# Performance work log

Hardware: AMD Instinct MI355X
Metric: run time of the kernel (lower is better)

Reference implementation:

```python
import jax, jax.numpy as jnp
import numpy as np

NUM_HEADS = 16
ROPE_THETA = 10000.0


def setup_inputs() -> dict:
    key = jax.random.key(0)
    k1, k2, k3 = jax.random.split(key, 3)
    B, S, D = 2, 2048, 1024
    std_qkv = float(np.sqrt(2.0 / (D + 3 * D)))
    std_out = float(np.sqrt(2.0 / (D + D)))
    return {
        "x": jax.random.normal(k1, (B, S, D), dtype=jnp.float32),
        "qkv_w": jax.random.normal(k2, (3 * D, D), dtype=jnp.float32) * std_qkv,
        "out_w": jax.random.normal(k3, (D, D), dtype=jnp.float32) * std_out,
        "token_positions": jnp.arange(S, dtype=jnp.int32),
    }


def _apply_rope(x, token_positions, theta=ROPE_THETA):
    # x: [B, H, S, d_k], token_positions: [S]
    d_k = x.shape[-1]
    inv_freqs = 1.0 / (theta ** (jnp.arange(0, d_k, 2, dtype=jnp.float32) / d_k))  # [d_k/2]
    angles = token_positions.astype(jnp.float32)[:, None] * inv_freqs[None, :]     # [S, d_k/2]
    cos, sin = jnp.cos(angles), jnp.sin(angles)
    x_even, x_odd = x[..., 0::2], x[..., 1::2]
    r_even = x_even * cos - x_odd * sin
    r_odd = x_even * sin + x_odd * cos
    # interleave back: [..., d_k/2, 2] -> [..., d_k]
    return jnp.stack([r_even, r_odd], axis=-1).reshape(x.shape)


def reference(x, qkv_w, out_w, token_positions):
    B, S, D = x.shape
    H = NUM_HEADS
    d_k = D // H

    qkv = jnp.einsum("bsd,ed->bse", x, qkv_w)                  # [B, S, 3*D]
    qkv = qkv.reshape(B, S, 3, H, d_k)
    q, k, v = (jnp.transpose(qkv[:, :, i], (0, 2, 1, 3)) for i in range(3))  # each [B, H, S, d_k]

    q = _apply_rope(q, token_positions)
    k = _apply_rope(k, token_positions)

    scale = 1.0 / jnp.sqrt(jnp.asarray(d_k, dtype=x.dtype))
    scores = jnp.einsum("bhqd,bhkd->bhqk", q, k) * scale       # [B, H, S, S]
    causal = jnp.tril(jnp.ones((S, S), dtype=bool))
    scores = jnp.where(causal, scores, jnp.asarray(-jnp.inf, dtype=scores.dtype))
    attn = jax.nn.softmax(scores, axis=-1)
    out = jnp.einsum("bhqk,bhkd->bhqd", attn, v)               # [B, H, S, d_k]
    out = jnp.transpose(out, (0, 2, 1, 3)).reshape(B, S, D)    # [B, S, D]
    return jnp.einsum("bsd,ed->bse", out, out_w)               # [B, S, D]
```

## Files before the change

### kernel.cpp

```cpp
#include <hip/hip_runtime.h>

typedef __bf16 bf16x8 __attribute__((ext_vector_type(8)));
typedef float f32x4 __attribute__((ext_vector_type(4)));
typedef unsigned short u16;
typedef u16 u16x8 __attribute__((ext_vector_type(8)));
typedef u16 u16x2 __attribute__((ext_vector_type(2)));

__device__ __forceinline__ u16 f2bf(float f) {
    union { float f; unsigned u; } x; x.f = f;
    unsigned r = x.u + 0x7fffu + ((x.u >> 16) & 1u);
    return (u16)(r >> 16);
}
__device__ __forceinline__ float bf2f(u16 v) {
    union { unsigned u; float f; } x; x.u = ((unsigned)v) << 16;
    return x.f;
}
__device__ __forceinline__ bf16x8 as_bf16x8(u16x8 v) {
    return __builtin_bit_cast(bf16x8, v);
}
__device__ __forceinline__ void glds16(const void* g, void* l) {
    __builtin_amdgcn_global_load_lds(
        (const __attribute__((address_space(1))) void*)g,
        (__attribute__((address_space(3))) void*)l, 16, 0, 0);
}
__device__ __forceinline__ int swz(int r) { return (((r & 7) ^ ((r >> 3) & 7)) << 3); }

__global__ __launch_bounds__(256) void cvt3(const float* __restrict__ x,
                                            const float* __restrict__ w,
                                            const float* __restrict__ ow,
                                            u16* __restrict__ x16,
                                            u16* __restrict__ w16,
                                            u16* __restrict__ ow16) {
    int i = blockIdx.x * 256 + threadIdx.x;
    const float* in; u16* out; int off;
    if (i < 524288)       { in = x;  out = x16;  off = i; }
    else if (i < 917504)  { in = w;  out = w16;  off = i - 524288; }
    else                  { in = ow; out = ow16; off = i - 917504; }
    const float4* p = (const float4*)(in + (size_t)off * 8);
    float4 a = p[0], b = p[1];
    u16x8 o;
    o[0] = f2bf(a.x); o[1] = f2bf(a.y); o[2] = f2bf(a.z); o[3] = f2bf(a.w);
    o[4] = f2bf(b.x); o[5] = f2bf(b.y); o[6] = f2bf(b.z); o[7] = f2bf(b.w);
    *(u16x8*)(out + (size_t)off * 8) = o;
}

__global__ __launch_bounds__(256) void gemm_qkv(const u16* __restrict__ A,
                                                const u16* __restrict__ B,
                                                u16* __restrict__ Qb,
                                                u16* __restrict__ Kb,
                                                u16* __restrict__ Vraw) {
    __shared__ u16 As[2][4096];
    __shared__ u16 Bs[2][4096];
    const int K = 1024, nbx = 24;
    const int tid = threadIdx.x, lane = tid & 63, wave = tid >> 6;
    const int cpx = gridDim.x >> 3;
    const int nid = (blockIdx.x & 7) * cpx + (blockIdx.x >> 3);
    const int m0 = (nid / nbx) << 7, n0 = (nid % nbx) << 7;
    const int wr = (wave >> 1) << 6, wc = (wave & 1) << 6;
    const int fr = lane & 15, fo = (lane >> 4) << 3;
    const int srow = tid >> 2, scol = (tid & 3) << 3;
    const u16* Ag = A + (size_t)(m0 + srow) * K + scol;
    const u16* Bg = B + (size_t)(n0 + srow) * K + scol;
    u16* AsW = &As[0][0] + (wave << 9);
    u16* BsW = &Bs[0][0] + (wave << 9);
    f32x4 acc[4][4] = {};
    const int nsteps = K >> 5;
    glds16(Ag, AsW);
    glds16(Ag + (size_t)64 * K, AsW + 2048);
    glds16(Bg, BsW);
    glds16(Bg + (size_t)64 * K, BsW + 2048);
    int cur = 0;
    for (int s = 0; s < nsteps; ++s) {
        __syncthreads();
        if (s + 1 < nsteps) {
            const u16* Ap = Ag + (s + 1) * 32;
            const u16* Bp = Bg + (s + 1) * 32;
            const int nb = (cur ^ 1) << 12;
            glds16(Ap, AsW + nb);
            glds16(Ap + (size_t)64 * K, AsW + nb + 2048);
            glds16(Bp, BsW + nb);
            glds16(Bp + (size_t)64 * K, BsW + nb + 2048);
        }
        const u16* Ab = &As[cur][0];
        const u16* Bb = &Bs[cur][0];
        bf16x8 af[4], bfr[4];
        #pragma unroll
        for (int i = 0; i < 4; ++i)
            af[i] = *(const bf16x8*)(Ab + (wr + i * 16 + fr) * 32 + fo);
        #pragma unroll
        for (int i = 0; i < 4; ++i)
            bfr[i] = *(const bf16x8*)(Bb + (wc + i * 16 + fr) * 32 + fo);
        #pragma unroll
        for (int i = 0; i < 4; ++i)
            #pragma unroll
            for (int j = 0; j < 4; ++j)
                acc[i][j] = __builtin_amdgcn_mfma_f32_16x16x32_bf16(af[i], bfr[j], acc[i][j], 0, 0, 0);
        cur ^= 1;
    }
    const int cr = (lane >> 4) << 2, cc = lane & 15;
    if (n0 >= 2048) {
        #pragma unroll
        for (int i = 0; i < 4; ++i)
            for (int j = 0; j < 4; ++j)
                for (int r = 0; r < 4; ++r)
                    Vraw[(size_t)(m0 + wr + i * 16 + cr + r) * 1024 +
                         (n0 - 2048 + wc + j * 16 + cc)] = f2bf(acc[i][j][r]);
    } else {
        const bool isQ = (n0 < 1024);
        u16* const Out = isQ ? Qb : Kb;
        const float qs = isQ ? 0.18033688011112042f : 1.0f;
        const float sgn = (cc & 1) ? 1.f : -1.f;
        const int bb = m0 >> 11;
        const int s_base = (m0 & 2047) + wr + cr;
        #pragma unroll
        for (int j = 0; j < 4; ++j) {
            const int n = n0 + wc + j * 16 + cc;
            const int d = n & 63, h = (n >> 6) & 15;
            const float invf = exp2f((float)(d >> 1) * -0.4152410118609203f)
                             * 0.15915494309189535f;
            u16* const ob = Out + (((size_t)(bb * 16 + h)) << 17) + d;
            #pragma unroll
            for (int i = 0; i < 4; ++i) {
                #pragma unroll
                for (int r = 0; r < 4; ++r) {
                    const int s = s_base + i * 16 + r;
                    float own  = acc[i][j][r];
                    float part = __shfl_xor(own, 1);
                    float rev  = (float)s * invf;
                    rev -= floorf(rev);
                    float sn = __builtin_amdgcn_sinf(rev);
                    float cs = __builtin_amdgcn_cosf(rev);
                    float o  = (cs * own + sgn * sn * part) * qs;
                    ob[(size_t)s * 64] = f2bf(o);
                }
            }
        }
    }
}

__global__ __launch_bounds__(256) void gemm128(const u16* __restrict__ A,
                                               const u16* __restrict__ B,
                                               float* __restrict__ C,
                                               int N, int K, int nbx) {
    __shared__ u16 As[2][4096];
    __shared__ u16 Bs[2][4096];
    const int tid = threadIdx.x, lane = tid & 63, wave = tid >> 6;
    const int cpx = gridDim.x >> 3;
    const int nid = (blockIdx.x & 7) * cpx + (blockIdx.x >> 3);
    const int m0 = (nid / nbx) << 7, n0 = (nid % nbx) << 7;
    const int wr = (wave >> 1) << 6, wc = (wave & 1) << 6;
    const int fr = lane & 15, fo = (lane >> 4) << 3;
    const int srow = tid >> 2, scol = (tid & 3) << 3;
    const u16* Ag = A + (size_t)(m0 + srow) * K + scol;
    const u16* Bg = B + (size_t)(n0 + srow) * K + scol;
    u16* AsW = &As[0][0] + (wave << 9);
    u16* BsW = &Bs[0][0] + (wave << 9);
    f32x4 acc[4][4] = {};
    const int nsteps = K >> 5;
    glds16(Ag, AsW);
    glds16(Ag + (size_t)64 * K, AsW + 2048);
    glds16(Bg, BsW);
    glds16(Bg + (size_t)64 * K, BsW + 2048);
    int cur = 0;
    for (int s = 0; s < nsteps; ++s) {
        __syncthreads();
        if (s + 1 < nsteps) {
            const u16* Ap = Ag + (s + 1) * 32;
            const u16* Bp = Bg + (s + 1) * 32;
            const int nb = (cur ^ 1) << 12;
            glds16(Ap, AsW + nb);
            glds16(Ap + (size_t)64 * K, AsW + nb + 2048);
            glds16(Bp, BsW + nb);
            glds16(Bp + (size_t)64 * K, BsW + nb + 2048);
        }
        const u16* Ab = &As[cur][0];
        const u16* Bb = &Bs[cur][0];
        bf16x8 af[4], bfr[4];
        #pragma unroll
        for (int i = 0; i < 4; ++i)
            af[i] = *(const bf16x8*)(Ab + (wr + i * 16 + fr) * 32 + fo);
        #pragma unroll
        for (int i = 0; i < 4; ++i)
            bfr[i] = *(const bf16x8*)(Bb + (wc + i * 16 + fr) * 32 + fo);
        #pragma unroll
        for (int i = 0; i < 4; ++i)
            #pragma unroll
            for (int j = 0; j < 4; ++j)
                acc[i][j] = __builtin_amdgcn_mfma_f32_16x16x32_bf16(af[i], bfr[j], acc[i][j], 0, 0, 0);
        cur ^= 1;
    }
    const int cr = (lane >> 4) << 2, cc = lane & 15;
    #pragma unroll
    for (int i = 0; i < 4; ++i)
        for (int j = 0; j < 4; ++j)
            for (int r = 0; r < 4; ++r)
                C[(size_t)(m0 + wr + i * 16 + cr + r) * N + (n0 + wc + j * 16 + cc)] =
                    acc[i][j][r];
}

__global__ __launch_bounds__(256) void vtrans(const u16* __restrict__ Vraw,
                                              u16* __restrict__ Vt) {
    __shared__ u16 lds[64][72];
    const int t = threadIdx.x;
    const int st = blockIdx.x, h = blockIdx.y, b = blockIdx.z;
    const int s0 = st << 6;
    {
        const int r = t >> 2, c0 = (t & 3) << 4;
        const u16* src = Vraw + (size_t)((b << 11) + s0 + r) * 1024 + h * 64 + c0;
        *(u16x8*)&lds[r][c0]     = *(const u16x8*)src;
        *(u16x8*)&lds[r][c0 + 8] = *(const u16x8*)(src + 8);
    }
    __syncthreads();
    const size_t obase = ((size_t)((b << 4) + h) << 17) + (st << 6);
    #pragma unroll
    for (int w = 0; w < 2; ++w) {
        const int q = t + (w << 8);
        const int d = q >> 3, c = q & 7;
        u16x8 o;
        #pragma unroll
        for (int i = 0; i < 8; ++i) {
            const int p = (c << 3) + i;
            const int k = ((p >> 5) << 5) + (((p >> 3) & 3) << 2) + (p & 3)
                        + (((p >> 2) & 1) << 4);
            o[i] = lds[k][d];
        }
        *(u16x8*)(Vt + obase + ((size_t)d << 11) + (c << 3)) = o;
    }
}

__global__ __launch_bounds__(512, 4) void attn_causal(const u16* __restrict__ Q,
                                                      const u16* __restrict__ K,
                                                      const u16* __restrict__ Vt,
                                                      u16* __restrict__ O) {
    __shared__ u16 smem[24576];
    __shared__ float cmb[5120];
    const int tid = threadIdx.x, lane = tid & 63, wave = tid >> 6;
    const int nid = ((blockIdx.x & 7) << 6) + (blockIdx.x >> 3);
    const int pr = nid & 15, h = (nid >> 4) & 15, b = nid >> 8;
    const int S = 2048;
    const size_t base = (size_t)((b << 4) + h) << 17;
    const int fr = lane & 15, fo = (lane >> 4) << 3, cr = (lane >> 4) << 2;
    const int schk = lane & 7, srow8 = lane >> 3;
    const int qsub = wave >> 1, half = wave & 1;
    float* const slot = cmb + qsub * 1280 + lane * 20;
    u16x8 ones_u;
    #pragma unroll
    for (int i = 0; i < 8; ++i) ones_u[i] = 0x3F80;
    const bf16x8 ones = as_bf16x8(ones_u);

    auto stage = [&](int t, int bi) {
        const int r  = (wave << 3) + srow8;
        const int ck = (schk ^ srow8 ^ wave) << 3;
        glds16(K  + base + ((size_t)((t << 6) + r) << 6) + ck,
               &smem[bi * 8192 + (wave << 9)]);
        glds16(Vt + base + ((size_t)r << 11) + (t << 6) + ck,
               &smem[bi * 8192 + 4096 + (wave << 9)]);
    };

    for (int phase = 0; phase < 2; ++phase) {
        const int qt = phase ? (31 - pr) : pr;
        const int nkt = qt + 1;
        const int qw = (qt << 6) + (qsub << 4);
        bf16x8 aq0, aq1;
        {
            const u16* qrow = Q + base + (size_t)(qw + fr) * 64;
            aq0 = as_bf16x8(*(const u16x8*)(qrow + fo));
            aq1 = as_bf16x8(*(const u16x8*)(qrow + 32 + fo));
        }
        f32x4 oacc[4] = {};
        f32x4 lacc = {};
        const int qloc = (qsub << 4) + fr;
        stage(0, 0);
        if (nkt > 1) stage(1, 1);
        int cur = 0;
        for (int t = 0; t < nkt; ++t) {
            if (t + 1 < nkt) asm volatile("s_waitcnt vmcnt(2)" ::: "memory");
            else             asm volatile("s_waitcnt vmcnt(0)" ::: "memory");
            __builtin_amdgcn_s_barrier();
            __builtin_amdgcn_sched_barrier(0);
            int nb = cur + 2; if (nb >= 3) nb -= 3;
            if (t + 2 < nkt) stage(t + 2, nb);
            const u16* Kb = smem + cur * 8192;
            const u16* Vb = smem + cur * 8192 + 4096;
            const bool diag = (t == nkt - 1);
            f32x4 sacc[2];
            #pragma unroll
            for (int ch = 0; ch < 2; ++ch) {
                const int r = ((half << 1) + ch) * 16 + fr;
                const int sw = swz(r);
                bf16x8 bk0 = *(const bf16x8*)&Kb[r * 64 + (fo ^ sw)];
                bf16x8 bk1 = *(const bf16x8*)&Kb[r * 64 + ((32 + fo) ^ sw)];
                f32x4 sc = {};
                sc = __builtin_amdgcn_mfma_f32_16x16x32_bf16(bk0, aq0, sc, 0, 0, 0);
                sc = __builtin_amdgcn_mfma_f32_16x16x32_bf16(bk1, aq1, sc, 0, 0, 0);
                sacc[ch] = sc;
            }
            bf16x8 pa;
            #pragma unroll
            for (int ch = 0; ch < 2; ++ch) {
                const int cglob = (half << 1) + ch;
                #pragma unroll
                for (int r = 0; r < 4; ++r) {
                    float e = exp2f(sacc[ch][r]);
                    if (diag) {
                        const int kloc = (cglob << 4) + cr + r;
                        e = (kloc <= qloc) ? e : 0.f;
                    }
                    pa[ch * 4 + r] = (__bf16)e;
                }
            }
            lacc = __builtin_amdgcn_mfma_f32_16x16x32_bf16(pa, ones, lacc, 0, 0, 0);
            #pragma unroll
            for (int tt = 0; tt < 4; ++tt) {
                const int d = tt * 16 + fr;
                bf16x8 bv = *(const bf16x8*)&Vb[d * 64 + (((half << 5) + fo) ^ swz(d))];
                oacc[tt] = __builtin_amdgcn_mfma_f32_16x16x32_bf16(pa, bv, oacc[tt], 0, 0, 0);
            }
            cur = (cur + 1 == 3) ? 0 : cur + 1;
        }
        __syncthreads();
        if (half) {
            #pragma unroll
            for (int tt = 0; tt < 4; ++tt) *(f32x4*)(slot + tt * 4) = oacc[tt];
            *(f32x4*)(slot + 16) = lacc;
        }
        __syncthreads();
        if (!half) {
            #pragma unroll
            for (int tt = 0; tt < 4; ++tt) oacc[tt] += *(const f32x4*)(slot + tt * 4);
            lacc += *(const f32x4*)(slot + 16);
            f32x4 inv;
            #pragma unroll
            for (int j = 0; j < 4; ++j) inv[j] = 1.f / lacc[j];
            #pragma unroll
            for (int tt = 0; tt < 4; ++tt)
                for (int j = 0; j < 4; ++j)
                    O[(size_t)(b * S + qw + cr + j) * 1024 + h * 64 + tt * 16 + fr] =
                        f2bf(oacc[tt][j] * inv[j]);
        }
        __syncthreads();
    }
}

extern "C" void kernel_launch(void* const* d_in, const int* in_sizes, int n_in,
                              void* d_out, int out_size, void* d_ws, size_t ws_size,
                              hipStream_t stream) {
    const float* x     = (const float*)d_in[0];
    const float* qkv_w = (const float*)d_in[1];
    const float* out_w = (const float*)d_in[2];
    float* out = (float*)d_out;

    char* ws = (char*)d_ws;
    u16* Vraw  = (u16*)ws;
    u16* Qb    = (u16*)(ws + 25165824);
    u16* Kb    = (u16*)(ws + 33554432);
    u16* Vtg   = (u16*)(ws + 41943040);
    u16* x16   = (u16*)(ws + 50331648);
    u16* att16 = (u16*)(ws + 50331648);
    u16* w16   = (u16*)(ws + 58720256);
    u16* ow16  = (u16*)(ws + 65011712);

    cvt3<<<4096, 256, 0, stream>>>(x, qkv_w, out_w, x16, w16, ow16);
    gemm_qkv<<<768, 256, 0, stream>>>(x16, w16, Qb, Kb, Vraw);
    vtrans<<<dim3(32, 16, 2), 256, 0, stream>>>(Vraw, Vtg);
    attn_causal<<<512, 512, 0, stream>>>(Qb, Kb, Vtg, att16);
    gemm128<<<256, 256, 0, stream>>>(att16, ow16, out, 1024, 1024, 8);
}
```

Baseline: 134.7 us.

## Fuse V transpose into QKV GEMM epilogue via LDS staging, add MFMA priority hints

The QKV GEMM epilogue now stages its output tile in shared memory and writes Q/K rows and the transposed, permuted V layout with 16-byte vector stores. This removes the separate vtrans kernel and its round trip through a raw V buffer, and replaces the scattered 2-byte global stores. The attention kernel also raises wave priority around its MFMA sections with s_setprio. The cost is a larger LDS footprint and extra barriers in the GEMM epilogue. The gemm128 kernel gains a template for bf16 output that is not used.

Result: faster. 115.4 us (-14.3%).

```diff
diff --git a/kernel.cpp b/kernel.cpp
--- a/kernel.cpp
+++ b/kernel.cpp
@@ -4,6 +4,7 @@
 typedef float f32x4 __attribute__((ext_vector_type(4)));
 typedef unsigned short u16;
 typedef u16 u16x8 __attribute__((ext_vector_type(8)));
+typedef u16 u16x4 __attribute__((ext_vector_type(4)));
 typedef u16 u16x2 __attribute__((ext_vector_type(2)));
 
 __device__ __forceinline__ u16 f2bf(float f) {
@@ -48,9 +49,8 @@
                                                 const u16* __restrict__ B,
                                                 u16* __restrict__ Qb,
                                                 u16* __restrict__ Kb,
-                                                u16* __restrict__ Vraw) {
-    __shared__ u16 As[2][4096];
-    __shared__ u16 Bs[2][4096];
+                                                u16* __restrict__ Vt) {
+    __shared__ u16 smem[17408];
     const int K = 1024, nbx = 24;
     const int tid = threadIdx.x, lane = tid & 63, wave = tid >> 6;
     const int cpx = gridDim.x >> 3;
@@ -61,8 +61,8 @@
     const int srow = tid >> 2, scol = (tid & 3) << 3;
     const u16* Ag = A + (size_t)(m0 + srow) * K + scol;
     const u16* Bg = B + (size_t)(n0 + srow) * K + scol;
-    u16* AsW = &As[0][0] + (wave << 9);
-    u16* BsW = &Bs[0][0] + (wave << 9);
+    u16* AsW = smem + (wave << 9);
+    u16* BsW = smem + 8192 + (wave << 9);
     f32x4 acc[4][4] = {};
     const int nsteps = K >> 5;
     glds16(Ag, AsW);
@@ -81,8 +81,8 @@
             glds16(Bp, BsW + nb);
             glds16(Bp + (size_t)64 * K, BsW + nb + 2048);
         }
-        const u16* Ab = &As[cur][0];
-        const u16* Bb = &Bs[cur][0];
+        const u16* Ab = smem + (cur << 12);
+        const u16* Bb = smem + 8192 + (cur << 12);
         bf16x8 af[4], bfr[4];
         #pragma unroll
         for (int i = 0; i < 4; ++i)
@@ -98,49 +98,76 @@
         cur ^= 1;
     }
     const int cr = (lane >> 4) << 2, cc = lane & 15;
+    const int bb = m0 >> 11, sb = m0 & 2047;
+    __syncthreads();
     if (n0 >= 2048) {
         #pragma unroll
-        for (int i = 0; i < 4; ++i)
-            for (int j = 0; j < 4; ++j)
-                for (int r = 0; r < 4; ++r)
-                    Vraw[(size_t)(m0 + wr + i * 16 + cr + r) * 1024 +
-                         (n0 - 2048 + wc + j * 16 + cc)] = f2bf(acc[i][j][r]);
+        for (int i = 0; i < 4; ++i) {
+            const int sl = wr + i * 16 + cr;
+            const int k = sl & 63;
+            const int p0 = ((sl >> 6) << 6) + ((k >> 5) << 5) + (((k >> 2) & 3) << 3)
+                         + (((k >> 4) & 1) << 2);
+            #pragma unroll
+            for (int j = 0; j < 4; ++j) {
+                const int c = wc + j * 16 + cc;
+                u16x4 v4;
+                #pragma unroll
+                for (int r = 0; r < 4; ++r) v4[r] = f2bf(acc[i][j][r]);
+                *(u16x4*)&smem[c * 136 + p0] = v4;
+            }
+        }
+        __syncthreads();
+        const int c = tid >> 1, hf = tid & 1;
+        const int hh = c >> 6, d = c & 63;
+        const int h0 = (n0 - 2048) >> 6;
+        u16* dst = Vt + (((size_t)(bb * 16 + h0 + hh)) << 17) + ((size_t)d << 11)
+                 + sb + (hf << 6);
+        const u16* sr = &smem[c * 136 + (hf << 6)];
+        #pragma unroll
+        for (int q = 0; q < 8; ++q)
+            *(u16x8*)(dst + q * 8) = *(const u16x8*)(sr + q * 8);
     } else {
         const bool isQ = (n0 < 1024);
-        u16* const Out = isQ ? Qb : Kb;
         const float qs = isQ ? 0.18033688011112042f : 1.0f;
         const float sgn = (cc & 1) ? 1.f : -1.f;
-        const int bb = m0 >> 11;
-        const int s_base = (m0 & 2047) + wr + cr;
         #pragma unroll
         for (int j = 0; j < 4; ++j) {
-            const int n = n0 + wc + j * 16 + cc;
-            const int d = n & 63, h = (n >> 6) & 15;
-            const float invf = exp2f((float)(d >> 1) * -0.4152410118609203f)
+            const int c = wc + j * 16 + cc;
+            const int tr = (c & 63) >> 1;
+            const float invf = exp2f((float)tr * -0.4152410118609203f)
                              * 0.15915494309189535f;
-            u16* const ob = Out + (((size_t)(bb * 16 + h)) << 17) + d;
             #pragma unroll
             for (int i = 0; i < 4; ++i) {
                 #pragma unroll
                 for (int r = 0; r < 4; ++r) {
-                    const int s = s_base + i * 16 + r;
+                    const int sl = wr + i * 16 + cr + r;
                     float own  = acc[i][j][r];
                     float part = __shfl_xor(own, 1);
-                    float rev  = (float)s * invf;
+                    float rev  = (float)(sb + sl) * invf;
                     rev -= floorf(rev);
                     float sn = __builtin_amdgcn_sinf(rev);
                     float cs = __builtin_amdgcn_cosf(rev);
-                    float o  = (cs * own + sgn * sn * part) * qs;
-                    ob[(size_t)s * 64] = f2bf(o);
+                    smem[sl * 136 + c] = f2bf((cs * own + sgn * sn * part) * qs);
                 }
             }
         }
-    }
-}
-
+        __syncthreads();
+        const int sl = tid >> 1, hh = tid & 1;
+        const int h0 = (isQ ? n0 : (n0 - 1024)) >> 6;
+        u16* Outb = isQ ? Qb : Kb;
+        u16* dst = Outb + (((size_t)(bb * 16 + h0 + hh)) << 17)
+                 + ((size_t)(sb + sl) << 6);
+        const u16* sr = &smem[sl * 136 + (hh << 6)];
+        #pragma unroll
+        for (int q = 0; q < 8; ++q)
+            *(u16x8*)(dst + q * 8) = *(const u16x8*)(sr + q * 8);
+    }
+}
+
+template<bool BF16OUT>
 __global__ __launch_bounds__(256) void gemm128(const u16* __restrict__ A,
                                                const u16* __restrict__ B,
-                                               float* __restrict__ C,
+                                               void* __restrict__ Cv,
                                                int N, int K, int nbx) {
     __shared__ u16 As[2][4096];
     __shared__ u16 Bs[2][4096];
@@ -190,41 +217,22 @@
         cur ^= 1;
     }
     const int cr = (lane >> 4) << 2, cc = lane & 15;
-    #pragma unroll
-    for (int i = 0; i < 4; ++i)
-        for (int j = 0; j < 4; ++j)
-            for (int r = 0; r < 4; ++r)
-                C[(size_t)(m0 + wr + i * 16 + cr + r) * N + (n0 + wc + j * 16 + cc)] =
-                    acc[i][j][r];
-}
-
-__global__ __launch_bounds__(256) void vtrans(const u16* __restrict__ Vraw,
-                                              u16* __restrict__ Vt) {
-    __shared__ u16 lds[64][72];
-    const int t = threadIdx.x;
-    const int st = blockIdx.x, h = blockIdx.y, b = blockIdx.z;
-    const int s0 = st << 6;
-    {
-        const int r = t >> 2, c0 = (t & 3) << 4;
-        const u16* src = Vraw + (size_t)((b << 11) + s0 + r) * 1024 + h * 64 + c0;
-        *(u16x8*)&lds[r][c0]     = *(const u16x8*)src;
-        *(u16x8*)&lds[r][c0 + 8] = *(const u16x8*)(src + 8);
-    }
-    __syncthreads();
-    const size_t obase = ((size_t)((b << 4) + h) << 17) + (st << 6);
-    #pragma unroll
-    for (int w = 0; w < 2; ++w) {
-        const int q = t + (w << 8);
-        const int d = q >> 3, c = q & 7;
-        u16x8 o;
-        #pragma unroll
-        for (int i = 0; i < 8; ++i) {
-            const int p = (c << 3) + i;
-            const int k = ((p >> 5) << 5) + (((p >> 3) & 3) << 2) + (p & 3)
-                        + (((p >> 2) & 1) << 4);
-            o[i] = lds[k][d];
-        }
-        *(u16x8*)(Vt + obase + ((size_t)d << 11) + (c << 3)) = o;
+    if constexpr (BF16OUT) {
+        u16* C = (u16*)Cv;
+        #pragma unroll
+        for (int i = 0; i < 4; ++i)
+            for (int j = 0; j < 4; ++j)
+                for (int r = 0; r < 4; ++r)
+                    C[(size_t)(m0 + wr + i * 16 + cr + r) * N + (n0 + wc + j * 16 + cc)] =
+                        f2bf(acc[i][j][r]);
+    } else {
+        float* C = (float*)Cv;
+        #pragma unroll
+        for (int i = 0; i < 4; ++i)
+            for (int j = 0; j < 4; ++j)
+                for (int r = 0; r < 4; ++r)
+                    C[(size_t)(m0 + wr + i * 16 + cr + r) * N + (n0 + wc + j * 16 + cc)] =
+                        acc[i][j][r];
     }
 }
 
@@ -284,6 +292,7 @@
             const u16* Vb = smem + cur * 8192 + 4096;
             const bool diag = (t == nkt - 1);
             f32x4 sacc[2];
+            __builtin_amdgcn_s_setprio(1);
             #pragma unroll
             for (int ch = 0; ch < 2; ++ch) {
                 const int r = ((half << 1) + ch) * 16 + fr;
@@ -295,6 +304,7 @@
                 sc = __builtin_amdgcn_mfma_f32_16x16x32_bf16(bk1, aq1, sc, 0, 0, 0);
                 sacc[ch] = sc;
             }
+            __builtin_amdgcn_s_setprio(0);
             bf16x8 pa;
             #pragma unroll
             for (int ch = 0; ch < 2; ++ch) {
@@ -309,6 +319,7 @@
                     pa[ch * 4 + r] = (__bf16)e;
                 }
             }
+            __builtin_amdgcn_s_setprio(1);
             lacc = __builtin_amdgcn_mfma_f32_16x16x32_bf16(pa, ones, lacc, 0, 0, 0);
             #pragma unroll
             for (int tt = 0; tt < 4; ++tt) {
@@ -316,6 +327,7 @@
                 bf16x8 bv = *(const bf16x8*)&Vb[d * 64 + (((half << 5) + fo) ^ swz(d))];
                 oacc[tt] = __builtin_amdgcn_mfma_f32_16x16x32_bf16(pa, bv, oacc[tt], 0, 0, 0);
             }
+            __builtin_amdgcn_s_setprio(0);
             cur = (cur + 1 == 3) ? 0 : cur + 1;
         }
         __syncthreads();
@@ -351,7 +363,6 @@
     float* out = (float*)d_out;
 
     char* ws = (char*)d_ws;
-    u16* Vraw  = (u16*)ws;
     u16* Qb    = (u16*)(ws + 25165824);
     u16* Kb    = (u16*)(ws + 33554432);
     u16* Vtg   = (u16*)(ws + 41943040);
@@ -361,8 +372,7 @@
     u16* ow16  = (u16*)(ws + 65011712);
 
     cvt3<<<4096, 256, 0, stream>>>(x, qkv_w, out_w, x16, w16, ow16);
-    gemm_qkv<<<768, 256, 0, stream>>>(x16, w16, Qb, Kb, Vraw);
-    vtrans<<<dim3(32, 16, 2), 256, 0, stream>>>(Vraw, Vtg);
+    gemm_qkv<<<768, 256, 0, stream>>>(x16, w16, Qb, Kb, Vtg);
     attn_causal<<<512, 512, 0, stream>>>(Qb, Kb, Vtg, att16);
-    gemm128<<<256, 256, 0, stream>>>(att16, ow16, out, 1024, 1024, 8);
-}
+    gemm128<false><<<256, 256, 0, stream>>>(att16, ow16, (void*)out, 1024, 1024, 8);
+}
```
